# Kernel tuning notes

Hardware: AMD Instinct MI355X
Metric: run time of the kernel (lower is better)

Reference implementation:

```python
import jax, jax.numpy as jnp
import numpy as np

N, CDIM, FDIM, HDIM, K = 16384, 512, 512, 1024, 5
WEIGHT = 5.0
EPS = 1e-20


def _xavier(key, shape, gain):
    fan_in, fan_out = shape[-2], shape[-1]
    std = gain * np.sqrt(2.0 / (fan_in + fan_out))
    return jax.random.normal(key, shape, jnp.float32) * std


def setup_inputs() -> dict:
    key = jax.random.key(0)
    ks = jax.random.split(key, 12)
    g = np.sqrt(2.0)  # relu gain; last layer linear gain=1
    inp = {
        "c": jax.random.normal(ks[0], (N, CDIM), jnp.float32),
        "x": jax.random.normal(ks[1], (N, 3), jnp.float32),
        "noise": jax.random.normal(ks[2], (K, N, FDIM), jnp.float32),
        "gumbel_u": jax.random.uniform(ks[3], (N, K), jnp.float32),
        # probs MLP: cdim -> 1024 -> 1024 -> K
        "pw0": _xavier(ks[4], (CDIM, HDIM), g), "pb0": jnp.zeros((HDIM,), jnp.float32),
        "pw1": _xavier(ks[5], (HDIM, HDIM), g), "pb1": jnp.zeros((HDIM,), jnp.float32),
        "pw2": _xavier(ks[6], (HDIM, K), 1.0), "pb2": jnp.zeros((K,), jnp.float32),
        # K Gaussian MLPs (stacked): cdim -> 1024 -> 1024 -> 2*fdim
        "gw0": _xavier(ks[7], (K, CDIM, HDIM), g), "gb0": jnp.zeros((K, HDIM), jnp.float32),
        "gw1": _xavier(ks[8], (K, HDIM, HDIM), g), "gb1": jnp.zeros((K, HDIM), jnp.float32),
        "gw2": _xavier(ks[9], (K, HDIM, 2 * FDIM), 1.0), "gb2": jnp.zeros((K, 2 * FDIM), jnp.float32),
    }
    return inp


def reference(c, x, noise, gumbel_u, pw0, pb0, pw1, pb1, pw2, pb2,
              gw0, gb0, gw1, gb1, gw2, gb2):
    # mixture probabilities: ps = softmax(probs(c))
    h = jax.nn.relu(c @ pw0 + pb0)
    h = jax.nn.relu(h @ pw1 + pb1)
    logits = h @ pw2 + pb2                      # (N, K)
    ps = jax.nn.softmax(logits, axis=-1)

    # all K Gaussian experts, vectorized over component axis k
    g = jax.nn.relu(jnp.einsum('nc,kch->knh', c, gw0) + gb0[:, None, :])
    g = jax.nn.relu(jnp.einsum('knh,khj->knj', g, gw1) + gb1[:, None, :])
    o = jnp.einsum('knh,khf->knf', g, gw2) + gb2[:, None, :]   # (K, N, 2*FDIM)
    mean, logvar = o[..., :FDIM], o[..., FDIM:]
    sample = mean + noise * jnp.exp(logvar * 0.5)              # (K, N, FDIM)

    # per-row categorical draw with p = ps (Gumbel-max, on-device)
    gumbel = -jnp.log(-jnp.log(gumbel_u + EPS) + EPS)
    idx = jnp.argmax(jnp.log(jax.lax.stop_gradient(ps) + EPS) + gumbel, axis=-1)

    mask = jax.nn.one_hot(idx, K, dtype=ps.dtype) * WEIGHT
    weights = (ps + mask) / (1.0 + WEIGHT)                     # (N, K)
    out = jnp.einsum('nk,knf->nf', weights, sample)            # (N, FDIM)
    return out
```

## Files before the change

### kernel.cpp

```cpp
#include <hip/hip_runtime.h>
#include <cstdint>
#include <cstddef>

#define N_ROWS 16384
#define CDIM_C 512
#define HDIM_C 1024
#define FDIM_C 512
#define KMIX 5

typedef unsigned short u16;
typedef __attribute__((ext_vector_type(8))) short bf16x8;
typedef __attribute__((ext_vector_type(4))) float f32x4;

__device__ __forceinline__ u16 f2bf(float x) {
  unsigned u = __float_as_uint(x);
  unsigned r = (u + 0x7fffu + ((u >> 16) & 1u)) >> 16;
  return (u16)r;
}
__device__ __forceinline__ float bf2f(u16 h) {
  return __uint_as_float(((unsigned)h) << 16);
}

__device__ __forceinline__ void gload_lds16(const void* g, void* l) {
  __builtin_amdgcn_global_load_lds((const __attribute__((address_space(1))) void*)g,
                                   (__attribute__((address_space(3))) void*)l,
                                   16, 0, 0);
}

__global__ void split3_kernel(const float* __restrict__ x, u16* __restrict__ P0,
                              u16* __restrict__ P1, u16* __restrict__ P2, size_t n) {
  for (size_t i = (size_t)blockIdx.x * 256 + threadIdx.x; i < n; i += (size_t)gridDim.x * 256) {
    const float v = x[i];
    const u16 h = f2bf(v); const float hf = bf2f(h);
    const u16 m = f2bf(v - hf); const float mf = bf2f(m);
    P0[i] = h; P1[i] = m; P2[i] = f2bf(v - hf - mf);
  }
}

template <int NP, bool PERM>
__global__ void transp_split_kernel(const float* __restrict__ W, u16* __restrict__ P0,
                                    u16* __restrict__ P1, u16* __restrict__ P2,
                                    int R, int C) {
  __shared__ float t[32][33];
  const int bz = blockIdx.z;
  const float* Wz = W + (size_t)bz * R * C;
  const size_t oofs = (size_t)bz * R * C;
  const int r0 = blockIdx.x * 32, c0 = blockIdx.y * 32;
  const int tx = threadIdx.x, ty = threadIdx.y;
#pragma unroll
  for (int i = 0; i < 4; ++i)
    t[ty + i * 8][tx] = Wz[(size_t)(r0 + ty + i * 8) * C + c0 + tx];
  __syncthreads();
#pragma unroll
  for (int i = 0; i < 4; ++i) {
    const int c_raw = c0 + ty + i * 8, r = r0 + tx;
    const int c = PERM ? ((c_raw < FDIM_C) ? (c_raw * 2) : ((c_raw - FDIM_C) * 2 + 1)) : c_raw;
    const float x = t[tx][ty + i * 8];
    const size_t idx = oofs + (size_t)c * R + r;
    const u16 h = f2bf(x);
    P0[idx] = h;
    const float hf = bf2f(h);
    const u16 m = f2bf(x - hf);
    P1[idx] = m;
    if (NP >= 3) {
      const float mf = bf2f(m);
      P2[idx] = f2bf(x - hf - mf);
    }
  }
}

template <int NA, int NB, int NT, bool RELU, int OSPL, int MIX, int BPC>
__global__ __launch_bounds__(256, BPC) void gemm_split(
    const u16* __restrict__ A0, const u16* __restrict__ A1, const u16* __restrict__ A2,
    const u16* __restrict__ B0, const u16* __restrict__ B1, const u16* __restrict__ B2,
    const float* __restrict__ bias, float* __restrict__ outF,
    u16* __restrict__ O0, u16* __restrict__ O1, u16* __restrict__ O2,
    const float* __restrict__ noise_k, const float* __restrict__ wvec,
    float* __restrict__ mixout, int kidx,
    int M, int Nc, int Kd) {
  __shared__ u16 lds[(NA + NB) * 4096];
  const int tid = threadIdx.x;
  const int lane = tid & 63;
  const int wave = tid >> 6;
  const int wm = wave >> 1, wn = wave & 1;

  const int nwg = (int)(gridDim.x * gridDim.y);
  const int orig = (int)(blockIdx.y * gridDim.x + blockIdx.x);
  const int cpx = nwg >> 3;
  const int wg = (orig & 7) * cpx + (orig >> 3);
  const int col0 = (wg & 7) * 128;
  const int row0 = (wg >> 3) * 128;

  const u16* Ap[3] = {A0, A1, A2};
  const u16* Bp[3] = {B0, B1, B2};
  constexpr int TA[6] = {0, 0, 1, 1, 0, 2};
  constexpr int TB[6] = {0, 1, 0, 1, 2, 0};

  f32x4 acc[4][4] = {};
  const int kb = lane >> 4;
  const int rl = lane & 15;
  const int nSteps = Kd >> 5;

  for (int kt = 0; kt < nSteps; ++kt) {
    const int k0 = kt << 5;
    __syncthreads();
#pragma unroll
    for (int p = 0; p < NA + NB; ++p) {
      const u16* gp = (p < NA) ? Ap[p] : Bp[p - NA];
      const int rb = (p < NA) ? row0 : col0;
      u16* lbase = &lds[p * 4096];
#pragma unroll
      for (int it = 0; it < 2; ++it) {
        const int sbase = it * 256 + wave * 64;
        const int slot = sbase + lane;
        const int skb = slot >> 7;
        const int sr = slot & 127;
        const u16* src = gp + (size_t)(rb + sr) * Kd + (k0 + skb * 8);
        gload_lds16(src, lbase + sbase * 8);
      }
    }
    __syncthreads();

    bf16x8 aF[NA][4];
    bf16x8 bF[NB][4];
#pragma unroll
    for (int p = 0; p < NA; ++p)
#pragma unroll
      for (int i = 0; i < 4; ++i) {
        const int r = wm * 64 + i * 16 + rl;
        aF[p][i] = *(const bf16x8*)&lds[p * 4096 + (kb * 128 + r) * 8];
      }
#pragma unroll
    for (int p = 0; p < NB; ++p)
#pragma unroll
      for (int j = 0; j < 4; ++j) {
        const int r = wn * 64 + j * 16 + rl;
        bF[p][j] = *(const bf16x8*)&lds[(NA + p) * 4096 + (kb * 128 + r) * 8];
      }
#pragma unroll
    for (int t = 0; t < NT; ++t)
#pragma unroll
      for (int i = 0; i < 4; ++i)
#pragma unroll
        for (int j = 0; j < 4; ++j)
          acc[i][j] = __builtin_amdgcn_mfma_f32_16x16x32_bf16(
              aF[TA[t]][i], bF[TB[t]][j], acc[i][j], 0, 0, 0);
  }

#pragma unroll
  for (int i = 0; i < 4; ++i)
#pragma unroll
    for (int j = 0; j < 4; ++j)
#pragma unroll
      for (int r = 0; r < 4; ++r) {
        const int row = row0 + wm * 64 + i * 16 + (lane >> 4) * 4 + r;
        const int col = col0 + wn * 64 + j * 16 + (lane & 15);
        if constexpr (MIX > 0) {
          const int f = col >> 1;
          const int ocol = (col & 1) ? (f + FDIM_C) : f;
          const float y = acc[i][j][r] + bias[ocol];
          const float other = __shfl_xor(y, 1);
          if (!(lane & 1)) {
            const float sample = y + noise_k[(size_t)row * FDIM_C + f] * expf(0.5f * other);
            const float v = wvec[row * KMIX + kidx] * sample;
            float* op = &mixout[(size_t)row * FDIM_C + f];
            if constexpr (MIX == 1) *op = v; else *op += v;
          }
        } else {
          float y = acc[i][j][r] + bias[col];
          if (RELU) y = fmaxf(y, 0.0f);
          const size_t idx = (size_t)row * Nc + col;
          if constexpr (OSPL == 0) {
            outF[idx] = y;
          } else {
            const u16 h = f2bf(y);
            const float hf = bf2f(h);
            const u16 m = f2bf(y - hf);
            O0[idx] = h;
            O1[idx] = m;
            if constexpr (OSPL == 3) {
              const float mf = bf2f(m);
              O2[idx] = f2bf(y - hf - mf);
            }
          }
        }
      }
  (void)M;
}

__global__ void p2_weights_kernel(const float* __restrict__ h2, const float* __restrict__ pw2,
                                  const float* __restrict__ pb2, const float* __restrict__ gu,
                                  float* __restrict__ w) {
  const int n = blockIdx.x * 4 + (threadIdx.x >> 6);
  const int lane = threadIdx.x & 63;
  const float* hrow = h2 + (size_t)n * HDIM_C;
  double acc[KMIX] = {0, 0, 0, 0, 0};
  const int c0 = lane * 16;
#pragma unroll
  for (int jj = 0; jj < 16; ++jj) {
    const int cc = c0 + jj;
    const double hv = (double)hrow[cc];
#pragma unroll
    for (int kk = 0; kk < KMIX; ++kk)
      acc[kk] += hv * (double)pw2[cc * KMIX + kk];
  }
#pragma unroll
  for (int offs = 32; offs >= 1; offs >>= 1)
#pragma unroll
    for (int kk = 0; kk < KMIX; ++kk)
      acc[kk] += __shfl_down(acc[kk], offs);
  if (lane == 0) {
    double lg[KMIX], mx = -1e300;
#pragma unroll
    for (int kk = 0; kk < KMIX; ++kk) {
      lg[kk] = acc[kk] + (double)pb2[kk];
      if (lg[kk] > mx) mx = lg[kk];
    }
    double e[KMIX], s = 0.0;
#pragma unroll
    for (int kk = 0; kk < KMIX; ++kk) { e[kk] = exp(lg[kk] - mx); s += e[kk]; }
    int idx = 0; double zb = -1e300;
#pragma unroll
    for (int kk = 0; kk < KMIX; ++kk) {
      const double ps = e[kk] / s;
      const double u = (double)gu[n * KMIX + kk];
      const double g = -log(-log(u + 1e-20) + 1e-20);
      const double zz = log(ps + 1e-20) + g;
      if (zz > zb) { zb = zz; idx = kk; }
    }
#pragma unroll
    for (int kk = 0; kk < KMIX; ++kk)
      w[n * KMIX + kk] = (float)((e[kk] / s + (kk == idx ? 5.0 : 0.0)) / 6.0);
  }
}

extern "C" void kernel_launch(void* const* d_in, const int* in_sizes, int n_in,
                              void* d_out, int out_size, void* d_ws, size_t ws_size,
                              hipStream_t stream) {
  const float* c   = (const float*)d_in[0];
  const float* noise = (const float*)d_in[2];
  const float* gu  = (const float*)d_in[3];
  const float* pw0 = (const float*)d_in[4];
  const float* pb0 = (const float*)d_in[5];
  const float* pw1 = (const float*)d_in[6];
  const float* pb1 = (const float*)d_in[7];
  const float* pw2 = (const float*)d_in[8];
  const float* pb2 = (const float*)d_in[9];
  const float* gw0 = (const float*)d_in[10];
  const float* gb0 = (const float*)d_in[11];
  const float* gw1 = (const float*)d_in[12];
  const float* gb1 = (const float*)d_in[13];
  const float* gw2 = (const float*)d_in[14];
  const float* gb2 = (const float*)d_in[15];
  float* out = (float*)d_out;

  char* ws = (char*)d_ws;
  size_t off = 0;
  auto alloc = [&](size_t bytes) -> char* {
    off = (off + 255) & ~(size_t)255;
    char* p = ws + off;
    off += bytes;
    return p;
  };

  const size_t NCp = (size_t)N_ROWS * CDIM_C * 2;
  const size_t NHp = (size_t)N_ROWS * HDIM_C * 2;
  u16* cH = (u16*)alloc(NCp);
  u16* cM = (u16*)alloc(NCp);
  u16* cL = (u16*)alloc(NCp);
  u16* pw0T0 = (u16*)alloc((size_t)CDIM_C * HDIM_C * 2);
  u16* pw0T1 = (u16*)alloc((size_t)CDIM_C * HDIM_C * 2);
  u16* pw0T2 = (u16*)alloc((size_t)CDIM_C * HDIM_C * 2);
  u16* pw1T0 = (u16*)alloc((size_t)HDIM_C * HDIM_C * 2);
  u16* pw1T1 = (u16*)alloc((size_t)HDIM_C * HDIM_C * 2);
  u16* pw1T2 = (u16*)alloc((size_t)HDIM_C * HDIM_C * 2);
  u16* hH = (u16*)alloc(NHp);
  u16* hM = (u16*)alloc(NHp);
  u16* hL = (u16*)alloc(NHp);
  float* h2 = (float*)alloc((size_t)N_ROWS * HDIM_C * 4);
  float* wbuf = (float*)alloc((size_t)N_ROWS * KMIX * 4);
  u16* gw0T0 = (u16*)alloc((size_t)KMIX * CDIM_C * HDIM_C * 2);
  u16* gw0T1 = (u16*)alloc((size_t)KMIX * CDIM_C * HDIM_C * 2);
  u16* gw1T0 = (u16*)alloc((size_t)KMIX * HDIM_C * HDIM_C * 2);
  u16* gw1T1 = (u16*)alloc((size_t)KMIX * HDIM_C * HDIM_C * 2);
  u16* gw2T0 = (u16*)alloc((size_t)KMIX * HDIM_C * HDIM_C * 2);
  u16* gw2T1 = (u16*)alloc((size_t)KMIX * HDIM_C * HDIM_C * 2);
  u16* g2b = (u16*)alloc(NHp);
  u16* g1a = hH;
  u16* g1b = hM;
  u16* g2a = hL;
  (void)ws_size; (void)in_sizes; (void)n_in; (void)out_size;

  split3_kernel<<<2048, 256, 0, stream>>>(c, cH, cM, cL, (size_t)N_ROWS * CDIM_C);
  transp_split_kernel<3, false><<<dim3(CDIM_C / 32, HDIM_C / 32, 1), dim3(32, 8), 0, stream>>>(
      pw0, pw0T0, pw0T1, pw0T2, CDIM_C, HDIM_C);
  transp_split_kernel<3, false><<<dim3(HDIM_C / 32, HDIM_C / 32, 1), dim3(32, 8), 0, stream>>>(
      pw1, pw1T0, pw1T1, pw1T2, HDIM_C, HDIM_C);
  transp_split_kernel<2, false><<<dim3(CDIM_C / 32, HDIM_C / 32, KMIX), dim3(32, 8), 0, stream>>>(
      gw0, gw0T0, gw0T1, nullptr, CDIM_C, HDIM_C);
  transp_split_kernel<2, false><<<dim3(HDIM_C / 32, HDIM_C / 32, KMIX), dim3(32, 8), 0, stream>>>(
      gw1, gw1T0, gw1T1, nullptr, HDIM_C, HDIM_C);
  transp_split_kernel<2, true><<<dim3(HDIM_C / 32, HDIM_C / 32, KMIX), dim3(32, 8), 0, stream>>>(
      gw2, gw2T0, gw2T1, nullptr, HDIM_C, HDIM_C);

  const dim3 gg(HDIM_C / 128, N_ROWS / 128);

  gemm_split<3, 3, 6, true, 3, 0, 3><<<gg, 256, 0, stream>>>(
      cH, cM, cL, pw0T0, pw0T1, pw0T2, pb0, nullptr, hH, hM, hL,
      nullptr, nullptr, nullptr, 0, N_ROWS, HDIM_C, CDIM_C);
  gemm_split<3, 3, 6, true, 0, 0, 3><<<gg, 256, 0, stream>>>(
      hH, hM, hL, pw1T0, pw1T1, pw1T2, pb1, h2, nullptr, nullptr, nullptr,
      nullptr, nullptr, nullptr, 0, N_ROWS, HDIM_C, HDIM_C);
  p2_weights_kernel<<<N_ROWS / 4, 256, 0, stream>>>(h2, pw2, pb2, gu, wbuf);

  for (int k = 0; k < KMIX; ++k) {
    gemm_split<2, 2, 3, true, 2, 0, 4><<<gg, 256, 0, stream>>>(
        cH, cM, nullptr,
        gw0T0 + (size_t)k * CDIM_C * HDIM_C, gw0T1 + (size_t)k * CDIM_C * HDIM_C, nullptr,
        gb0 + k * HDIM_C, nullptr, g1a, g1b, nullptr,
        nullptr, nullptr, nullptr, 0, N_ROWS, HDIM_C, CDIM_C);
    gemm_split<2, 2, 3, true, 2, 0, 4><<<gg, 256, 0, stream>>>(
        g1a, g1b, nullptr,
        gw1T0 + (size_t)k * HDIM_C * HDIM_C, gw1T1 + (size_t)k * HDIM_C * HDIM_C, nullptr,
        gb1 + k * HDIM_C, nullptr, g2a, g2b, nullptr,
        nullptr, nullptr, nullptr, 0, N_ROWS, HDIM_C, HDIM_C);
    if (k == 0)
      gemm_split<2, 2, 3, false, 0, 1, 4><<<gg, 256, 0, stream>>>(
          g2a, g2b, nullptr,
          gw2T0 + (size_t)k * HDIM_C * HDIM_C, gw2T1 + (size_t)k * HDIM_C * HDIM_C, nullptr,
          gb2 + k * HDIM_C, nullptr, nullptr, nullptr, nullptr,
          noise + (size_t)k * N_ROWS * FDIM_C, wbuf, out, k, N_ROWS, HDIM_C, HDIM_C);
    else
      gemm_split<2, 2, 3, false, 0, 2, 4><<<gg, 256, 0, stream>>>(
          g2a, g2b, nullptr,
          gw2T0 + (size_t)k * HDIM_C * HDIM_C, gw2T1 + (size_t)k * HDIM_C * HDIM_C, nullptr,
          gb2 + k * HDIM_C, nullptr, nullptr, nullptr, nullptr,
          noise + (size_t)k * N_ROWS * FDIM_C, wbuf, out, k, N_ROWS, HDIM_C, HDIM_C);
  }
}
```

Baseline: 2.470 ms.

## Replace split-bf16 GEMM with 256x256 double-buffered pipelined kernel over split planes

Replaces the 128x128, 4-wave split-precision GEMM with a 256x256-tile, 8-wave kernel. The kernel double-buffers 64-wide K slices in LDS via direct global-to-LDS loads and interleaves the next tile's loads with MFMA phases, using explicit waitcnt, barriers and setprio. The bf16 split-plane products are no longer loaded and multiplied together per K step. Instead each plane pair becomes its own segment of a longer, linearised K loop. The aim is more operand reuse per byte fetched and loads hidden behind compute. In exchange the kernel uses 128 KB of LDS, has more register pressure, and relies on hand-tuned synchronisation that could race or stall.

```diff
diff --git a/kernel.cpp b/kernel.cpp
--- a/kernel.cpp
+++ b/kernel.cpp
@@ -21,7 +21,7 @@
   return __uint_as_float(((unsigned)h) << 16);
 }
 
-__device__ __forceinline__ void gload_lds16(const void* g, void* l) {
+__device__ __forceinline__ void gload_lds16(const u16* g, u16* l) {
   __builtin_amdgcn_global_load_lds((const __attribute__((address_space(1))) void*)g,
                                    (__attribute__((address_space(3))) void*)l,
                                    16, 0, 0);
@@ -69,96 +69,163 @@
   }
 }
 
-template <int NA, int NB, int NT, bool RELU, int OSPL, int MIX, int BPC>
-__global__ __launch_bounds__(256, BPC) void gemm_split(
+template <int NT, bool RELU, int OSPL, int MIX>
+__global__ __launch_bounds__(512, 2) void gemm256(
     const u16* __restrict__ A0, const u16* __restrict__ A1, const u16* __restrict__ A2,
     const u16* __restrict__ B0, const u16* __restrict__ B1, const u16* __restrict__ B2,
     const float* __restrict__ bias, float* __restrict__ outF,
     u16* __restrict__ O0, u16* __restrict__ O1, u16* __restrict__ O2,
     const float* __restrict__ noise_k, const float* __restrict__ wvec,
     float* __restrict__ mixout, int kidx,
-    int M, int Nc, int Kd) {
-  __shared__ u16 lds[(NA + NB) * 4096];
+    int Kd, int kpsl, int ntiles) {
+  __shared__ __align__(16) u16 lds[65536];
   const int tid = threadIdx.x;
   const int lane = tid & 63;
   const int wave = tid >> 6;
-  const int wm = wave >> 1, wn = wave & 1;
-
-  const int nwg = (int)(gridDim.x * gridDim.y);
-  const int orig = (int)(blockIdx.y * gridDim.x + blockIdx.x);
-  const int cpx = nwg >> 3;
-  const int wg = (orig & 7) * cpx + (orig >> 3);
-  const int col0 = (wg & 7) * 128;
-  const int row0 = (wg >> 3) * 128;
-
-  const u16* Ap[3] = {A0, A1, A2};
-  const u16* Bp[3] = {B0, B1, B2};
-  constexpr int TA[6] = {0, 0, 1, 1, 0, 2};
-  constexpr int TB[6] = {0, 1, 0, 1, 2, 0};
-
-  f32x4 acc[4][4] = {};
-  const int kb = lane >> 4;
-  const int rl = lane & 15;
-  const int nSteps = Kd >> 5;
-
-  for (int kt = 0; kt < nSteps; ++kt) {
-    const int k0 = kt << 5;
-    __syncthreads();
-#pragma unroll
-    for (int p = 0; p < NA + NB; ++p) {
-      const u16* gp = (p < NA) ? Ap[p] : Bp[p - NA];
-      const int rb = (p < NA) ? row0 : col0;
-      u16* lbase = &lds[p * 4096];
-#pragma unroll
-      for (int it = 0; it < 2; ++it) {
-        const int sbase = it * 256 + wave * 64;
-        const int slot = sbase + lane;
-        const int skb = slot >> 7;
-        const int sr = slot & 127;
-        const u16* src = gp + (size_t)(rb + sr) * Kd + (k0 + skb * 8);
-        gload_lds16(src, lbase + sbase * 8);
-      }
+  const int wm = wave >> 2, wn = wave & 3;
+  const int hi2 = tid >> 8, row_s = tid & 255;
+  const int kmask = (1 << kpsl) - 1;
+
+  const int orig = (int)(blockIdx.y * 4 + blockIdx.x);
+  const int wg = (orig & 7) * 32 + (orig >> 3);
+  const int col0 = (wg & 3) << 8;
+  const int row0 = (wg >> 2) << 8;
+
+  auto planes = [&](int kt, const u16*& pa, const u16*& pb, int& ko) {
+    const int seg = kt >> kpsl;
+    ko = (kt & kmask) << 6;
+    if constexpr (NT == 3) {
+      pa = (seg == 2) ? A1 : A0;
+      pb = (seg == 1) ? B1 : B0;
+    } else {
+      pa = (seg == 2 || seg == 3) ? A1 : ((seg == 5) ? A2 : A0);
+      pb = (seg == 1 || seg == 3) ? B1 : ((seg == 4) ? B2 : B0);
     }
-    __syncthreads();
-
-    bf16x8 aF[NA][4];
-    bf16x8 bF[NB][4];
-#pragma unroll
-    for (int p = 0; p < NA; ++p)
-#pragma unroll
-      for (int i = 0; i < 4; ++i) {
-        const int r = wm * 64 + i * 16 + rl;
-        aF[p][i] = *(const bf16x8*)&lds[p * 4096 + (kb * 128 + r) * 8];
-      }
-#pragma unroll
-    for (int p = 0; p < NB; ++p)
-#pragma unroll
-      for (int j = 0; j < 4; ++j) {
-        const int r = wn * 64 + j * 16 + rl;
-        bF[p][j] = *(const bf16x8*)&lds[(NA + p) * 4096 + (kb * 128 + r) * 8];
-      }
-#pragma unroll
-    for (int t = 0; t < NT; ++t)
-#pragma unroll
-      for (int i = 0; i < 4; ++i)
-#pragma unroll
-        for (int j = 0; j < 4; ++j)
-          acc[i][j] = __builtin_amdgcn_mfma_f32_16x16x32_bf16(
-              aF[TA[t]][i], bF[TB[t]][j], acc[i][j], 0, 0, 0);
-  }
-
-#pragma unroll
-  for (int i = 0; i < 4; ++i)
-#pragma unroll
-    for (int j = 0; j < 4; ++j)
+  };
+
+  auto stage = [&](int h, const u16* pa, const u16* pb, int ko, int db) {
+    const bool isA = ((h & 1) == 0);
+    const int kh = h >> 1;
+    const u16* base = isA ? pa : pb;
+    const int rb = isA ? row0 : col0;
+    const int ldsoff = db * 32768 + (isA ? 0 : 16384);
+#pragma unroll
+    for (int it = 0; it < 2; ++it) {
+      const u16* src = base + (size_t)(rb + row_s) * Kd + ko + (kh * 4 + it * 2 + hi2) * 8;
+      gload_lds16(src, &lds[ldsoff + (kh * 1024 + it * 512 + wave * 64) * 8]);
+    }
+  };
+
+  auto rdA = [&](int fm, int ks, int db) -> bf16x8 {
+    const int kb = ks * 4 + (lane >> 4);
+    const int r = wm * 128 + fm * 16 + (lane & 15);
+    return *(const bf16x8*)&lds[db * 32768 + kb * 2048 + r * 8];
+  };
+  auto rdB = [&](int fn, int ks, int db) -> bf16x8 {
+    const int kb = ks * 4 + (lane >> 4);
+    const int r = wn * 64 + fn * 16 + (lane & 15);
+    return *(const bf16x8*)&lds[db * 32768 + 16384 + kb * 2048 + r * 8];
+  };
+
+  f32x4 acc[8][4] = {};
+
+  {
+    const u16 *pa, *pb; int ko;
+    planes(0, pa, pb, ko);
+    stage(0, pa, pb, ko, 0); stage(1, pa, pb, ko, 0);
+    stage(2, pa, pb, ko, 0); stage(3, pa, pb, ko, 0);
+    asm volatile("s_waitcnt vmcnt(4)" ::: "memory");
+    __builtin_amdgcn_s_barrier();
+  }
+
+  for (int kt = 0; kt < ntiles; ++kt) {
+    const int cb = kt & 1, nb = cb ^ 1;
+    const bool notlast = (kt + 1 < ntiles);
+    const u16 *npa = A0, *npb = B0; int nko = 0;
+    if (notlast) planes(kt + 1, npa, npb, nko);
+    bf16x8 aR[4], bR[4];
+
+#pragma unroll
+    for (int fn = 0; fn < 4; ++fn) bR[fn] = rdB(fn, 0, cb);
+#pragma unroll
+    for (int fm = 0; fm < 4; ++fm) aR[fm] = rdA(fm, 0, cb);
+    if (notlast) stage(0, npa, npb, nko, nb);
+    __builtin_amdgcn_s_barrier();
+    asm volatile("s_waitcnt lgkmcnt(0)" ::: "memory");
+    __builtin_amdgcn_sched_barrier(0);
+    __builtin_amdgcn_s_setprio(1);
+#pragma unroll
+    for (int fm = 0; fm < 4; ++fm)
+#pragma unroll
+      for (int fn = 0; fn < 4; ++fn)
+        acc[fm][fn] = __builtin_amdgcn_mfma_f32_16x16x32_bf16(aR[fm], bR[fn], acc[fm][fn], 0, 0, 0);
+    __builtin_amdgcn_s_setprio(0);
+    __builtin_amdgcn_s_barrier();
+
+#pragma unroll
+    for (int fm = 0; fm < 4; ++fm) aR[fm] = rdA(4 + fm, 0, cb);
+    if (notlast) stage(1, npa, npb, nko, nb);
+    __builtin_amdgcn_s_barrier();
+    asm volatile("s_waitcnt lgkmcnt(0)" ::: "memory");
+    __builtin_amdgcn_sched_barrier(0);
+    __builtin_amdgcn_s_setprio(1);
+#pragma unroll
+    for (int fm = 0; fm < 4; ++fm)
+#pragma unroll
+      for (int fn = 0; fn < 4; ++fn)
+        acc[4 + fm][fn] = __builtin_amdgcn_mfma_f32_16x16x32_bf16(aR[fm], bR[fn], acc[4 + fm][fn], 0, 0, 0);
+    __builtin_amdgcn_s_setprio(0);
+    if (notlast) { asm volatile("s_waitcnt vmcnt(4)" ::: "memory"); }
+    else         { asm volatile("s_waitcnt vmcnt(0)" ::: "memory"); }
+    __builtin_amdgcn_s_barrier();
+
+#pragma unroll
+    for (int fn = 0; fn < 4; ++fn) bR[fn] = rdB(fn, 1, cb);
+#pragma unroll
+    for (int fm = 0; fm < 4; ++fm) aR[fm] = rdA(fm, 1, cb);
+    if (notlast) stage(2, npa, npb, nko, nb);
+    __builtin_amdgcn_s_barrier();
+    asm volatile("s_waitcnt lgkmcnt(0)" ::: "memory");
+    __builtin_amdgcn_sched_barrier(0);
+    __builtin_amdgcn_s_setprio(1);
+#pragma unroll
+    for (int fm = 0; fm < 4; ++fm)
+#pragma unroll
+      for (int fn = 0; fn < 4; ++fn)
+        acc[fm][fn] = __builtin_amdgcn_mfma_f32_16x16x32_bf16(aR[fm], bR[fn], acc[fm][fn], 0, 0, 0);
+    __builtin_amdgcn_s_setprio(0);
+    __builtin_amdgcn_s_barrier();
+
+#pragma unroll
+    for (int fm = 0; fm < 4; ++fm) aR[fm] = rdA(4 + fm, 1, cb);
+    if (notlast) stage(3, npa, npb, nko, nb);
+    __builtin_amdgcn_s_barrier();
+    asm volatile("s_waitcnt lgkmcnt(0)" ::: "memory");
+    __builtin_amdgcn_sched_barrier(0);
+    __builtin_amdgcn_s_setprio(1);
+#pragma unroll
+    for (int fm = 0; fm < 4; ++fm)
+#pragma unroll
+      for (int fn = 0; fn < 4; ++fn)
+        acc[4 + fm][fn] = __builtin_amdgcn_mfma_f32_16x16x32_bf16(aR[fm], bR[fn], acc[4 + fm][fn], 0, 0, 0);
+    __builtin_amdgcn_s_setprio(0);
+    if (notlast) { asm volatile("s_waitcnt vmcnt(4)" ::: "memory"); }
+    __builtin_amdgcn_s_barrier();
+  }
+
+  const int hi4 = lane >> 4, rl = lane & 15;
+#pragma unroll
+  for (int fm = 0; fm < 8; ++fm)
+#pragma unroll
+    for (int fn = 0; fn < 4; ++fn)
 #pragma unroll
       for (int r = 0; r < 4; ++r) {
-        const int row = row0 + wm * 64 + i * 16 + (lane >> 4) * 4 + r;
-        const int col = col0 + wn * 64 + j * 16 + (lane & 15);
+        const int row = row0 + wm * 128 + fm * 16 + hi4 * 4 + r;
+        const int col = col0 + wn * 64 + fn * 16 + rl;
         if constexpr (MIX > 0) {
           const int f = col >> 1;
           const int ocol = (col & 1) ? (f + FDIM_C) : f;
-          const float y = acc[i][j][r] + bias[ocol];
+          const float y = acc[fm][fn][r] + bias[ocol];
           const float other = __shfl_xor(y, 1);
           if (!(lane & 1)) {
             const float sample = y + noise_k[(size_t)row * FDIM_C + f] * expf(0.5f * other);
@@ -167,9 +234,9 @@
             if constexpr (MIX == 1) *op = v; else *op += v;
           }
         } else {
-          float y = acc[i][j][r] + bias[col];
+          float y = acc[fm][fn][r] + bias[col];
           if (RELU) y = fmaxf(y, 0.0f);
-          const size_t idx = (size_t)row * Nc + col;
+          const size_t idx = (size_t)row * HDIM_C + col;
           if constexpr (OSPL == 0) {
             outF[idx] = y;
           } else {
@@ -185,7 +252,6 @@
           }
         }
       }
-  (void)M;
 }
 
 __global__ void p2_weights_kernel(const float* __restrict__ h2, const float* __restrict__ pw2,
@@ -303,38 +369,38 @@
   transp_split_kernel<2, true><<<dim3(HDIM_C / 32, HDIM_C / 32, KMIX), dim3(32, 8), 0, stream>>>(
       gw2, gw2T0, gw2T1, nullptr, HDIM_C, HDIM_C);
 
-  const dim3 gg(HDIM_C / 128, N_ROWS / 128);
-
-  gemm_split<3, 3, 6, true, 3, 0, 3><<<gg, 256, 0, stream>>>(
+  const dim3 gg(HDIM_C / 256, N_ROWS / 256);
+
+  gemm256<6, true, 3, 0><<<gg, 512, 0, stream>>>(
       cH, cM, cL, pw0T0, pw0T1, pw0T2, pb0, nullptr, hH, hM, hL,
-      nullptr, nullptr, nullptr, 0, N_ROWS, HDIM_C, CDIM_C);
-  gemm_split<3, 3, 6, true, 0, 0, 3><<<gg, 256, 0, stream>>>(
+      nullptr, nullptr, nullptr, 0, CDIM_C, 3, 48);
+  gemm256<6, true, 0, 0><<<gg, 512, 0, stream>>>(
       hH, hM, hL, pw1T0, pw1T1, pw1T2, pb1, h2, nullptr, nullptr, nullptr,
-      nullptr, nullptr, nullptr, 0, N_ROWS, HDIM_C, HDIM_C);
+      nullptr, nullptr, nullptr, 0, HDIM_C, 4, 96);
   p2_weights_kernel<<<N_ROWS / 4, 256, 0, stream>>>(h2, pw2, pb2, gu, wbuf);
 
   for (int k = 0; k < KMIX; ++k) {
-    gemm_split<2, 2, 3, true, 2, 0, 4><<<gg, 256, 0, stream>>>(
+    gemm256<3, true, 2, 0><<<gg, 512, 0, stream>>>(
         cH, cM, nullptr,
         gw0T0 + (size_t)k * CDIM_C * HDIM_C, gw0T1 + (size_t)k * CDIM_C * HDIM_C, nullptr,
         gb0 + k * HDIM_C, nullptr, g1a, g1b, nullptr,
-        nullptr, nullptr, nullptr, 0, N_ROWS, HDIM_C, CDIM_C);
-    gemm_split<2, 2, 3, true, 2, 0, 4><<<gg, 256, 0, stream>>>(
+        nullptr, nullptr, nullptr, 0, CDIM_C, 3, 24);
+    gemm256<3, true, 2, 0><<<gg, 512, 0, stream>>>(
         g1a, g1b, nullptr,
         gw1T0 + (size_t)k * HDIM_C * HDIM_C, gw1T1 + (size_t)k * HDIM_C * HDIM_C, nullptr,
         gb1 + k * HDIM_C, nullptr, g2a, g2b, nullptr,
-        nullptr, nullptr, nullptr, 0, N_ROWS, HDIM_C, HDIM_C);
+        nullptr, nullptr, nullptr, 0, HDIM_C, 4, 48);
     if (k == 0)
-      gemm_split<2, 2, 3, false, 0, 1, 4><<<gg, 256, 0, stream>>>(
+      gemm256<3, false, 0, 1><<<gg, 512, 0, stream>>>(
           g2a, g2b, nullptr,
           gw2T0 + (size_t)k * HDIM_C * HDIM_C, gw2T1 + (size_t)k * HDIM_C * HDIM_C, nullptr,
           gb2 + k * HDIM_C, nullptr, nullptr, nullptr, nullptr,
-          noise + (size_t)k * N_ROWS * FDIM_C, wbuf, out, k, N_ROWS, HDIM_C, HDIM_C);
+          noise + (size_t)k * N_ROWS * FDIM_C, wbuf, out, k, HDIM_C, 4, 48);
     else
-      gemm_split<2, 2, 3, false, 0, 2, 4><<<gg, 256, 0, stream>>>(
+      gemm256<3, false, 0, 2><<<gg, 512, 0, stream>>>(
           g2a, g2b, nullptr,
           gw2T0 + (size_t)k * HDIM_C * HDIM_C, gw2T1 + (size_t)k * HDIM_C * HDIM_C, nullptr,
           gb2 + k * HDIM_C, nullptr, nullptr, nullptr, nullptr,
-          noise + (size_t)k * N_ROWS * FDIM_C, wbuf, out, k, N_ROWS, HDIM_C, HDIM_C);
-  }
-}
+          noise + (size_t)k * N_ROWS * FDIM_C, wbuf, out, k, HDIM_C, 4, 48);
+  }
+}
```

Result: faster. 2.388 ms (-3.3%).

## Restructure split-bf16 GEMM to iterate over precision-pair segments with one A/B tile per step

Applied to the files above, without the earlier changes.

Each k-step used to load all split planes of A and B (up to 3+3) and issue NT MFMA products against them. Now each step loads a single A plane and a single B plane with a 64-wide K slice, and the precision-term pairs become sequential K segments selected by a segment index. This fixes LDS at 32KB for every instance and cuts fragment registers, which allows the 6-term GEMMs to run at 4 blocks per CU instead of 3. In exchange, plane tiles are reloaded once per product term rather than shared across terms, which raises global/L2 traffic.

```diff
diff --git a/kernel.cpp b/kernel.cpp
--- a/kernel.cpp
+++ b/kernel.cpp
@@ -21,7 +21,7 @@
   return __uint_as_float(((unsigned)h) << 16);
 }
 
-__device__ __forceinline__ void gload_lds16(const void* g, void* l) {
+__device__ __forceinline__ void gload_lds16(const u16* g, u16* l) {
   __builtin_amdgcn_global_load_lds((const __attribute__((address_space(1))) void*)g,
                                    (__attribute__((address_space(3))) void*)l,
                                    16, 0, 0);
@@ -69,20 +69,22 @@
   }
 }
 
-template <int NA, int NB, int NT, bool RELU, int OSPL, int MIX, int BPC>
-__global__ __launch_bounds__(256, BPC) void gemm_split(
+template <int NT, bool RELU, int OSPL, int MIX, int BPC>
+__global__ __launch_bounds__(256, BPC) void gemm128(
     const u16* __restrict__ A0, const u16* __restrict__ A1, const u16* __restrict__ A2,
     const u16* __restrict__ B0, const u16* __restrict__ B1, const u16* __restrict__ B2,
     const float* __restrict__ bias, float* __restrict__ outF,
     u16* __restrict__ O0, u16* __restrict__ O1, u16* __restrict__ O2,
     const float* __restrict__ noise_k, const float* __restrict__ wvec,
     float* __restrict__ mixout, int kidx,
-    int M, int Nc, int Kd) {
-  __shared__ u16 lds[(NA + NB) * 4096];
+    int Kd, int kpsl, int nsteps) {
+  __shared__ __align__(16) u16 lds[16384];
   const int tid = threadIdx.x;
   const int lane = tid & 63;
   const int wave = tid >> 6;
   const int wm = wave >> 1, wn = wave & 1;
+  const int hi4 = lane >> 4, rl = lane & 15;
+  const int kmask = (1 << kpsl) - 1;
 
   const int nwg = (int)(gridDim.x * gridDim.y);
   const int orig = (int)(blockIdx.y * gridDim.x + blockIdx.x);
@@ -91,60 +93,47 @@
   const int col0 = (wg & 7) * 128;
   const int row0 = (wg >> 3) * 128;
 
-  const u16* Ap[3] = {A0, A1, A2};
-  const u16* Bp[3] = {B0, B1, B2};
-  constexpr int TA[6] = {0, 0, 1, 1, 0, 2};
-  constexpr int TB[6] = {0, 1, 0, 1, 2, 0};
-
   f32x4 acc[4][4] = {};
-  const int kb = lane >> 4;
-  const int rl = lane & 15;
-  const int nSteps = Kd >> 5;
-
-  for (int kt = 0; kt < nSteps; ++kt) {
-    const int k0 = kt << 5;
+
+  for (int kt = 0; kt < nsteps; ++kt) {
+    const int seg = kt >> kpsl;
+    const int ko = (kt & kmask) << 6;
+    const u16 *pa, *pb;
+    if constexpr (NT == 3) {
+      pa = (seg == 2) ? A1 : A0;
+      pb = (seg == 1) ? B1 : B0;
+    } else {
+      pa = (seg == 2 || seg == 3) ? A1 : ((seg == 5) ? A2 : A0);
+      pb = (seg == 1 || seg == 3) ? B1 : ((seg == 4) ? B2 : B0);
+    }
+
     __syncthreads();
 #pragma unroll
-    for (int p = 0; p < NA + NB; ++p) {
-      const u16* gp = (p < NA) ? Ap[p] : Bp[p - NA];
-      const int rb = (p < NA) ? row0 : col0;
-      u16* lbase = &lds[p * 4096];
-#pragma unroll
-      for (int it = 0; it < 2; ++it) {
-        const int sbase = it * 256 + wave * 64;
-        const int slot = sbase + lane;
-        const int skb = slot >> 7;
-        const int sr = slot & 127;
-        const u16* src = gp + (size_t)(rb + sr) * Kd + (k0 + skb * 8);
-        gload_lds16(src, lbase + sbase * 8);
-      }
+    for (int it = 0; it < 4; ++it) {
+      const int sbase = it * 256 + (wave << 6);
+      const int slot = sbase + lane;
+      const int skb = slot >> 7, sr = slot & 127;
+      gload_lds16(pa + (size_t)(row0 + sr) * Kd + ko + skb * 8, &lds[sbase * 8]);
+      gload_lds16(pb + (size_t)(col0 + sr) * Kd + ko + skb * 8, &lds[8192 + sbase * 8]);
     }
     __syncthreads();
 
-    bf16x8 aF[NA][4];
-    bf16x8 bF[NB][4];
-#pragma unroll
-    for (int p = 0; p < NA; ++p)
-#pragma unroll
-      for (int i = 0; i < 4; ++i) {
-        const int r = wm * 64 + i * 16 + rl;
-        aF[p][i] = *(const bf16x8*)&lds[p * 4096 + (kb * 128 + r) * 8];
-      }
-#pragma unroll
-    for (int p = 0; p < NB; ++p)
-#pragma unroll
-      for (int j = 0; j < 4; ++j) {
-        const int r = wn * 64 + j * 16 + rl;
-        bF[p][j] = *(const bf16x8*)&lds[(NA + p) * 4096 + (kb * 128 + r) * 8];
-      }
-#pragma unroll
-    for (int t = 0; t < NT; ++t)
+#pragma unroll
+    for (int ks = 0; ks < 2; ++ks) {
+      bf16x8 aR[4], bR[4];
+      const int kb = ks * 4 + hi4;
 #pragma unroll
       for (int i = 0; i < 4; ++i)
+        aR[i] = *(const bf16x8*)&lds[kb * 1024 + (wm * 64 + i * 16 + rl) * 8];
+#pragma unroll
+      for (int j = 0; j < 4; ++j)
+        bR[j] = *(const bf16x8*)&lds[8192 + kb * 1024 + (wn * 64 + j * 16 + rl) * 8];
+#pragma unroll
+      for (int i = 0; i < 4; ++i)
 #pragma unroll
         for (int j = 0; j < 4; ++j)
-          acc[i][j] = __builtin_amdgcn_mfma_f32_16x16x32_bf16(
-              aF[TA[t]][i], bF[TB[t]][j], acc[i][j], 0, 0, 0);
+          acc[i][j] = __builtin_amdgcn_mfma_f32_16x16x32_bf16(aR[i], bR[j], acc[i][j], 0, 0, 0);
+    }
   }
 
 #pragma unroll
@@ -153,8 +142,8 @@
     for (int j = 0; j < 4; ++j)
 #pragma unroll
       for (int r = 0; r < 4; ++r) {
-        const int row = row0 + wm * 64 + i * 16 + (lane >> 4) * 4 + r;
-        const int col = col0 + wn * 64 + j * 16 + (lane & 15);
+        const int row = row0 + wm * 64 + i * 16 + hi4 * 4 + r;
+        const int col = col0 + wn * 64 + j * 16 + rl;
         if constexpr (MIX > 0) {
           const int f = col >> 1;
           const int ocol = (col & 1) ? (f + FDIM_C) : f;
@@ -169,7 +158,7 @@
         } else {
           float y = acc[i][j][r] + bias[col];
           if (RELU) y = fmaxf(y, 0.0f);
-          const size_t idx = (size_t)row * Nc + col;
+          const size_t idx = (size_t)row * HDIM_C + col;
           if constexpr (OSPL == 0) {
             outF[idx] = y;
           } else {
@@ -185,7 +174,6 @@
           }
         }
       }
-  (void)M;
 }
 
 __global__ void p2_weights_kernel(const float* __restrict__ h2, const float* __restrict__ pw2,
@@ -305,36 +293,36 @@
 
   const dim3 gg(HDIM_C / 128, N_ROWS / 128);
 
-  gemm_split<3, 3, 6, true, 3, 0, 3><<<gg, 256, 0, stream>>>(
+  gemm128<6, true, 3, 0, 4><<<gg, 256, 0, stream>>>(
       cH, cM, cL, pw0T0, pw0T1, pw0T2, pb0, nullptr, hH, hM, hL,
-      nullptr, nullptr, nullptr, 0, N_ROWS, HDIM_C, CDIM_C);
-  gemm_split<3, 3, 6, true, 0, 0, 3><<<gg, 256, 0, stream>>>(
+      nullptr, nullptr, nullptr, 0, CDIM_C, 3, 48);
+  gemm128<6, true, 0, 0, 4><<<gg, 256, 0, stream>>>(
       hH, hM, hL, pw1T0, pw1T1, pw1T2, pb1, h2, nullptr, nullptr, nullptr,
-      nullptr, nullptr, nullptr, 0, N_ROWS, HDIM_C, HDIM_C);
+      nullptr, nullptr, nullptr, 0, HDIM_C, 4, 96);
   p2_weights_kernel<<<N_ROWS / 4, 256, 0, stream>>>(h2, pw2, pb2, gu, wbuf);
 
   for (int k = 0; k < KMIX; ++k) {
-    gemm_split<2, 2, 3, true, 2, 0, 4><<<gg, 256, 0, stream>>>(
+    gemm128<3, true, 2, 0, 4><<<gg, 256, 0, stream>>>(
         cH, cM, nullptr,
         gw0T0 + (size_t)k * CDIM_C * HDIM_C, gw0T1 + (size_t)k * CDIM_C * HDIM_C, nullptr,
         gb0 + k * HDIM_C, nullptr, g1a, g1b, nullptr,
-        nullptr, nullptr, nullptr, 0, N_ROWS, HDIM_C, CDIM_C);
-    gemm_split<2, 2, 3, true, 2, 0, 4><<<gg, 256, 0, stream>>>(
+        nullptr, nullptr, nullptr, 0, CDIM_C, 3, 24);
+    gemm128<3, true, 2, 0, 4><<<gg, 256, 0, stream>>>(
         g1a, g1b, nullptr,
         gw1T0 + (size_t)k * HDIM_C * HDIM_C, gw1T1 + (size_t)k * HDIM_C * HDIM_C, nullptr,
         gb1 + k * HDIM_C, nullptr, g2a, g2b, nullptr,
-        nullptr, nullptr, nullptr, 0, N_ROWS, HDIM_C, HDIM_C);
+        nullptr, nullptr, nullptr, 0, HDIM_C, 4, 48);
     if (k == 0)
-      gemm_split<2, 2, 3, false, 0, 1, 4><<<gg, 256, 0, stream>>>(
+      gemm128<3, false, 0, 1, 4><<<gg, 256, 0, stream>>>(
           g2a, g2b, nullptr,
           gw2T0 + (size_t)k * HDIM_C * HDIM_C, gw2T1 + (size_t)k * HDIM_C * HDIM_C, nullptr,
           gb2 + k * HDIM_C, nullptr, nullptr, nullptr, nullptr,
-          noise + (size_t)k * N_ROWS * FDIM_C, wbuf, out, k, N_ROWS, HDIM_C, HDIM_C);
+          noise + (size_t)k * N_ROWS * FDIM_C, wbuf, out, k, HDIM_C, 4, 48);
     else
-      gemm_split<2, 2, 3, false, 0, 2, 4><<<gg, 256, 0, stream>>>(
+      gemm128<3, false, 0, 2, 4><<<gg, 256, 0, stream>>>(
           g2a, g2b, nullptr,
           gw2T0 + (size_t)k * HDIM_C * HDIM_C, gw2T1 + (size_t)k * HDIM_C * HDIM_C, nullptr,
           gb2 + k * HDIM_C, nullptr, nullptr, nullptr, nullptr,
-          noise + (size_t)k * N_ROWS * FDIM_C, wbuf, out, k, N_ROWS, HDIM_C, HDIM_C);
-  }
-}
+          noise + (size_t)k * N_ROWS * FDIM_C, wbuf, out, k, HDIM_C, 4, 48);
+  }
+}
```

After: 3.613 ms. +46.3%, slower.

## Add 256x128-tile GEMM kernel with fragment reuse for Gaussian expert layers

Applied to the files above, without the earlier changes.

Adds a gemm_wide kernel that computes 256x128 output tiles, with each wave holding an 8x4 accumulator block. It is used for the 15 per-expert two-part bf16 GEMMs, while the probability MLP keeps the old kernel. Within each k-step it orders the three split-product MFMA passes so that A and B register fragments are reused across terms, cutting LDS reads and global tile loads per FLOP. The cost is higher register pressure (occupancy drops to 2 blocks per CU), more LDS per block, and half as many workgroups.

```diff
diff --git a/kernel.cpp b/kernel.cpp
--- a/kernel.cpp
+++ b/kernel.cpp
@@ -21,7 +21,7 @@
   return __uint_as_float(((unsigned)h) << 16);
 }
 
-__device__ __forceinline__ void gload_lds16(const void* g, void* l) {
+__device__ __forceinline__ void gload_lds16(const u16* g, u16* l) {
   __builtin_amdgcn_global_load_lds((const __attribute__((address_space(1))) void*)g,
                                    (__attribute__((address_space(3))) void*)l,
                                    16, 0, 0);
@@ -69,15 +69,13 @@
   }
 }
 
-template <int NA, int NB, int NT, bool RELU, int OSPL, int MIX, int BPC>
+template <int NA, int NB, int NT, bool RELU, int OSPL, int BPC>
 __global__ __launch_bounds__(256, BPC) void gemm_split(
     const u16* __restrict__ A0, const u16* __restrict__ A1, const u16* __restrict__ A2,
     const u16* __restrict__ B0, const u16* __restrict__ B1, const u16* __restrict__ B2,
     const float* __restrict__ bias, float* __restrict__ outF,
     u16* __restrict__ O0, u16* __restrict__ O1, u16* __restrict__ O2,
-    const float* __restrict__ noise_k, const float* __restrict__ wvec,
-    float* __restrict__ mixout, int kidx,
-    int M, int Nc, int Kd) {
+    int Nc, int Kd) {
   __shared__ u16 lds[(NA + NB) * 4096];
   const int tid = threadIdx.x;
   const int lane = tid & 63;
@@ -115,8 +113,7 @@
         const int slot = sbase + lane;
         const int skb = slot >> 7;
         const int sr = slot & 127;
-        const u16* src = gp + (size_t)(rb + sr) * Kd + (k0 + skb * 8);
-        gload_lds16(src, lbase + sbase * 8);
+        gload_lds16(gp + (size_t)(rb + sr) * Kd + (k0 + skb * 8), lbase + sbase * 8);
       }
     }
     __syncthreads();
@@ -126,17 +123,13 @@
 #pragma unroll
     for (int p = 0; p < NA; ++p)
 #pragma unroll
-      for (int i = 0; i < 4; ++i) {
-        const int r = wm * 64 + i * 16 + rl;
-        aF[p][i] = *(const bf16x8*)&lds[p * 4096 + (kb * 128 + r) * 8];
-      }
+      for (int i = 0; i < 4; ++i)
+        aF[p][i] = *(const bf16x8*)&lds[p * 4096 + (kb * 128 + wm * 64 + i * 16 + rl) * 8];
 #pragma unroll
     for (int p = 0; p < NB; ++p)
 #pragma unroll
-      for (int j = 0; j < 4; ++j) {
-        const int r = wn * 64 + j * 16 + rl;
-        bF[p][j] = *(const bf16x8*)&lds[(NA + p) * 4096 + (kb * 128 + r) * 8];
-      }
+      for (int j = 0; j < 4; ++j)
+        bF[p][j] = *(const bf16x8*)&lds[(NA + p) * 4096 + (kb * 128 + wn * 64 + j * 16 + rl) * 8];
 #pragma unroll
     for (int t = 0; t < NT; ++t)
 #pragma unroll
@@ -155,6 +148,108 @@
       for (int r = 0; r < 4; ++r) {
         const int row = row0 + wm * 64 + i * 16 + (lane >> 4) * 4 + r;
         const int col = col0 + wn * 64 + j * 16 + (lane & 15);
+        float y = acc[i][j][r] + bias[col];
+        if (RELU) y = fmaxf(y, 0.0f);
+        const size_t idx = (size_t)row * Nc + col;
+        if constexpr (OSPL == 0) {
+          outF[idx] = y;
+        } else {
+          const u16 h = f2bf(y);
+          const float hf = bf2f(h);
+          const u16 m = f2bf(y - hf);
+          O0[idx] = h;
+          O1[idx] = m;
+          if constexpr (OSPL == 3) {
+            const float mf = bf2f(m);
+            O2[idx] = f2bf(y - hf - mf);
+          }
+        }
+      }
+}
+
+template <bool RELU, int OSPL, int MIX>
+__global__ __launch_bounds__(256, 2) void gemm_wide(
+    const u16* __restrict__ A0, const u16* __restrict__ A1,
+    const u16* __restrict__ B0, const u16* __restrict__ B1,
+    const float* __restrict__ bias, float* __restrict__ outF,
+    u16* __restrict__ O0, u16* __restrict__ O1,
+    const float* __restrict__ noise_k, const float* __restrict__ wvec,
+    float* __restrict__ mixout, int kidx, int Kd) {
+  __shared__ __align__(16) u16 lds[24576];
+  const int tid = threadIdx.x;
+  const int lane = tid & 63;
+  const int wave = tid >> 6;
+  const int wm = wave >> 1, wn = wave & 1;
+  const int hi4 = lane >> 4, rl = lane & 15;
+
+  const int nwg = (int)(gridDim.x * gridDim.y);
+  const int orig = (int)(blockIdx.y * gridDim.x + blockIdx.x);
+  const int cpx = nwg >> 3;
+  const int wg = (orig & 7) * cpx + (orig >> 3);
+  const int col0 = (wg & 7) * 128;
+  const int row0 = (wg >> 3) * 256;
+
+  const u16* Ap[2] = {A0, A1};
+  const u16* Bp[2] = {B0, B1};
+
+  f32x4 acc[8][4] = {};
+  bf16x8 aR[8], bR[4];
+  const int nSteps = Kd >> 5;
+
+  auto ldA = [&](int p) {
+#pragma unroll
+    for (int i = 0; i < 8; ++i)
+      aR[i] = *(const bf16x8*)&lds[p * 8192 + (hi4 * 256 + wm * 128 + i * 16 + rl) * 8];
+  };
+  auto ldB = [&](int q) {
+#pragma unroll
+    for (int j = 0; j < 4; ++j)
+      bR[j] = *(const bf16x8*)&lds[16384 + q * 4096 + (hi4 * 128 + wn * 64 + j * 16 + rl) * 8];
+  };
+  auto FMA = [&]() {
+#pragma unroll
+    for (int i = 0; i < 8; ++i)
+#pragma unroll
+      for (int j = 0; j < 4; ++j)
+        acc[i][j] = __builtin_amdgcn_mfma_f32_16x16x32_bf16(aR[i], bR[j], acc[i][j], 0, 0, 0);
+  };
+
+  for (int kt = 0; kt < nSteps; ++kt) {
+    const int ko = kt << 5;
+    __syncthreads();
+#pragma unroll
+    for (int p = 0; p < 2; ++p)
+#pragma unroll
+      for (int it = 0; it < 4; ++it) {
+        const int sbase = it * 256 + (wave << 6);
+        const int slot = sbase + lane;
+        gload_lds16(Ap[p] + (size_t)(row0 + (slot & 255)) * Kd + ko + (slot >> 8) * 8,
+                    &lds[p * 8192 + sbase * 8]);
+      }
+#pragma unroll
+    for (int q = 0; q < 2; ++q)
+#pragma unroll
+      for (int it = 0; it < 2; ++it) {
+        const int sbase = it * 256 + (wave << 6);
+        const int slot = sbase + lane;
+        gload_lds16(Bp[q] + (size_t)(col0 + (slot & 127)) * Kd + ko + (slot >> 7) * 8,
+                    &lds[16384 + q * 4096 + sbase * 8]);
+      }
+    __syncthreads();
+
+    ldA(1); ldB(0); FMA();
+    ldA(0);         FMA();
+    ldB(1);         FMA();
+  }
+
+#pragma unroll
+  for (int i = 0; i < 8; ++i)
+#pragma unroll
+    for (int j = 0; j < 4; ++j)
+#pragma unroll
+      for (int r = 0; r < 4; ++r) {
+        const int row = row0 + wm * 128 + i * 16 + hi4 * 4 + r;
+        const int col = col0 + wn * 64 + j * 16 + rl;
         if constexpr (MIX > 0) {
           const int f = col >> 1;
           const int ocol = (col & 1) ? (f + FDIM_C) : f;
@@ -169,23 +264,14 @@
         } else {
           float y = acc[i][j][r] + bias[col];
           if (RELU) y = fmaxf(y, 0.0f);
-          const size_t idx = (size_t)row * Nc + col;
-          if constexpr (OSPL == 0) {
-            outF[idx] = y;
-          } else {
-            const u16 h = f2bf(y);
-            const float hf = bf2f(h);
-            const u16 m = f2bf(y - hf);
-            O0[idx] = h;
-            O1[idx] = m;
-            if constexpr (OSPL == 3) {
-              const float mf = bf2f(m);
-              O2[idx] = f2bf(y - hf - mf);
-            }
-          }
+          const size_t idx = (size_t)row * HDIM_C + col;
+          const u16 h = f2bf(y);
+          const float hf = bf2f(h);
+          O0[idx] = h;
+          O1[idx] = f2bf(y - hf);
+          (void)outF;
         }
       }
-  (void)M;
 }
 
 __global__ void p2_weights_kernel(const float* __restrict__ h2, const float* __restrict__ pw2,
@@ -303,38 +389,37 @@
   transp_split_kernel<2, true><<<dim3(HDIM_C / 32, HDIM_C / 32, KMIX), dim3(32, 8), 0, stream>>>(
       gw2, gw2T0, gw2T1, nullptr, HDIM_C, HDIM_C);
 
-  const dim3 gg(HDIM_C / 128, N_ROWS / 128);
-
-  gemm_split<3, 3, 6, true, 3, 0, 3><<<gg, 256, 0, stream>>>(
-      cH, cM, cL, pw0T0, pw0T1, pw0T2, pb0, nullptr, hH, hM, hL,
-      nullptr, nullptr, nullptr, 0, N_ROWS, HDIM_C, CDIM_C);
-  gemm_split<3, 3, 6, true, 0, 0, 3><<<gg, 256, 0, stream>>>(
-      hH, hM, hL, pw1T0, pw1T1, pw1T2, pb1, h2, nullptr, nullptr, nullptr,
-      nullptr, nullptr, nullptr, 0, N_ROWS, HDIM_C, HDIM_C);
+  const dim3 ggP(HDIM_C / 128, N_ROWS / 128);
+  const dim3 ggG(HDIM_C / 128, N_ROWS / 256);
+
+  gemm_split<3, 3, 6, true, 3, 3><<<ggP, 256, 0, stream>>>(
+      cH, cM, cL, pw0T0, pw0T1, pw0T2, pb0, nullptr, hH, hM, hL, HDIM_C, CDIM_C);
+  gemm_split<3, 3, 6, true, 0, 3><<<ggP, 256, 0, stream>>>(
+      hH, hM, hL, pw1T0, pw1T1, pw1T2, pb1, h2, nullptr, nullptr, nullptr, HDIM_C, HDIM_C);
   p2_weights_kernel<<<N_ROWS / 4, 256, 0, stream>>>(h2, pw2, pb2, gu, wbuf);
 
   for (int k = 0; k < KMIX; ++k) {
-    gemm_split<2, 2, 3, true, 2, 0, 4><<<gg, 256, 0, stream>>>(
-        cH, cM, nullptr,
-        gw0T0 + (size_t)k * CDIM_C * HDIM_C, gw0T1 + (size_t)k * CDIM_C * HDIM_C, nullptr,
-        gb0 + k * HDIM_C, nullptr, g1a, g1b, nullptr,
-        nullptr, nullptr, nullptr, 0, N_ROWS, HDIM_C, CDIM_C);
-    gemm_split<2, 2, 3, true, 2, 0, 4><<<gg, 256, 0, stream>>>(
-        g1a, g1b, nullptr,
-        gw1T0 + (size_t)k * HDIM_C * HDIM_C, gw1T1 + (size_t)k * HDIM_C * HDIM_C, nullptr,
-        gb1 + k * HDIM_C, nullptr, g2a, g2b, nullptr,
-        nullptr, nullptr, nullptr, 0, N_ROWS, HDIM_C, HDIM_C);
+    gemm_wide<true, 2, 0><<<ggG, 256, 0, stream>>>(
+        cH, cM,
+        gw0T0 + (size_t)k * CDIM_C * HDIM_C, gw0T1 + (size_t)k * CDIM_C * HDIM_C,
+        gb0 + k * HDIM_C, nullptr, g1a, g1b,
+        nullptr, nullptr, nullptr, 0, CDIM_C);
+    gemm_wide<true, 2, 0><<<ggG, 256, 0, stream>>>(
+        g1a, g1b,
+        gw1T0 + (size_t)k * HDIM_C * HDIM_C, gw1T1 + (size_t)k * HDIM_C * HDIM_C,
+        gb1 + k * HDIM_C, nullptr, g2a, g2b,
+        nullptr, nullptr, nullptr, 0, HDIM_C);
     if (k == 0)
-      gemm_split<2, 2, 3, false, 0, 1, 4><<<gg, 256, 0, stream>>>(
-          g2a, g2b, nullptr,
-          gw2T0 + (size_t)k * HDIM_C * HDIM_C, gw2T1 + (size_t)k * HDIM_C * HDIM_C, nullptr,
-          gb2 + k * HDIM_C, nullptr, nullptr, nullptr, nullptr,
-          noise + (size_t)k * N_ROWS * FDIM_C, wbuf, out, k, N_ROWS, HDIM_C, HDIM_C);
+      gemm_wide<false, 0, 1><<<ggG, 256, 0, stream>>>(
+          g2a, g2b,
+          gw2T0 + (size_t)k * HDIM_C * HDIM_C, gw2T1 + (size_t)k * HDIM_C * HDIM_C,
+          gb2 + k * HDIM_C, nullptr, nullptr, nullptr,
+          noise + (size_t)k * N_ROWS * FDIM_C, wbuf, out, k, HDIM_C);
     else
-      gemm_split<2, 2, 3, false, 0, 2, 4><<<gg, 256, 0, stream>>>(
-          g2a, g2b, nullptr,
-          gw2T0 + (size_t)k * HDIM_C * HDIM_C, gw2T1 + (size_t)k * HDIM_C * HDIM_C, nullptr,
-          gb2 + k * HDIM_C, nullptr, nullptr, nullptr, nullptr,
-          noise + (size_t)k * N_ROWS * FDIM_C, wbuf, out, k, N_ROWS, HDIM_C, HDIM_C);
-  }
-}
+      gemm_wide<false, 0, 2><<<ggG, 256, 0, stream>>>(
+          g2a, g2b,
+          gw2T0 + (size_t)k * HDIM_C * HDIM_C, gw2T1 + (size_t)k * HDIM_C * HDIM_C,
+          gb2 + k * HDIM_C, nullptr, nullptr, nullptr,
+          noise + (size_t)k * N_ROWS * FDIM_C, wbuf, out, k, HDIM_C);
+  }
+}
```

After: 2.346 ms. 1.05x faster.
